# Performance work log

Measured on AMD Instinct MI355X. Metric: run time of the kernel, lower is better.

Reference implementation:

```python
import jax, jax.numpy as jnp
from jax import lax
import numpy as np

B, T, V, E, H, D, NH = 64, 121, 100000, 300, 256, 512, 3  # D = 2*H (BiLSTM output)


def setup_inputs() -> dict:
    key = jax.random.key(0)
    ks = jax.random.split(key, 24)
    s = 0.05
    n = lambda k, shp: (jax.random.normal(k, shp, dtype=jnp.float32) * s)
    return {
        'tokens': jax.random.randint(ks[0], (B, T), 0, V, dtype=jnp.int32),
        'lengths': jax.random.randint(ks[1], (B,), 1, T + 1, dtype=jnp.int32),
        'emb': n(ks[2], (V, E)),
        'Wx_f': n(ks[3], (E, 4 * H)), 'Wh_f': n(ks[4], (H, 4 * H)), 'b_f': jnp.zeros((4 * H,), jnp.float32),
        'Wx_b': n(ks[5], (E, 4 * H)), 'Wh_b': n(ks[6], (H, 4 * H)), 'b_b': jnp.zeros((4 * H,), jnp.float32),
        'W1': n(ks[7], (4 * D, E)), 'b1': jnp.zeros((E,), jnp.float32),
        'W2': n(ks[8], (E, 1)), 'b2': jnp.zeros((1,), jnp.float32),
        'Wr': n(ks[9], (D, D)), 'Ur': n(ks[10], (D, D)), 'br': jnp.zeros((D,), jnp.float32),
        'Wc': n(ks[11], (D, D)), 'Uc': n(ks[12], (D, D)), 'bc': jnp.zeros((D,), jnp.float32),
        'q': n(ks[13], (B, D)),
        'W_hops': n(ks[14], (NH, 3 * D, D)), 'b_hops': jnp.zeros((NH, D), jnp.float32),
        'Wo': n(ks[15], (2 * D, 1)), 'bo': jnp.zeros((1,), jnp.float32),
    }


def _lstm(x, Wx, Wh, b, reverse=False):
    # x: [B, T, E] -> outputs [B, T, H]
    xp = jnp.einsum('bte,eg->btg', x, Wx) + b  # precompute input projections
    def cell(carry, xt):
        h, c = carry
        g = xt + h @ Wh
        i, f, gg, o = jnp.split(g, 4, axis=-1)
        c = jax.nn.sigmoid(f) * c + jax.nn.sigmoid(i) * jnp.tanh(gg)
        h = jax.nn.sigmoid(o) * jnp.tanh(c)
        return (h, c), h
    h0 = jnp.zeros((x.shape[0], Wh.shape[0]), x.dtype)
    (_, _), ys = lax.scan(cell, (h0, h0), jnp.swapaxes(xp, 0, 1), reverse=reverse)
    return jnp.swapaxes(ys, 0, 1)


def _attention(facts, q, m, mask, W1, b1, W2, b2):
    # facts [B,T,D]; q,m [B,D] -> softmax attention [B,T] (masked by length)
    qe, me = q[:, None, :], m[:, None, :]
    z = jnp.concatenate([facts * qe, facts * me, jnp.abs(facts - qe), jnp.abs(facts - me)], axis=-1)
    h = jnp.tanh(jnp.einsum('btf,fe->bte', z, W1) + b1)
    s = (jnp.einsum('bte,eo->bto', h, W2) + b2)[..., 0]  # [B,T]
    s = jnp.where(mask, s, jnp.float32(-1e9))
    return jax.nn.softmax(s, axis=1)


def _attn_gru(facts, g, Wr, Ur, br, Wc, Uc, bc):
    # attention-gated GRU over time; episode = final state [B,D]
    def cell(h, inp):
        x, gt = inp
        r = jax.nn.sigmoid(x @ Wr + h @ Ur + br)
        hc = jnp.tanh(x @ Wc + r * (h @ Uc) + bc)
        h = gt[:, None] * hc + (1.0 - gt[:, None]) * h
        return h, None
    h0 = jnp.zeros_like(facts[:, 0])
    h, _ = lax.scan(cell, h0, (jnp.swapaxes(facts, 0, 1), g.T))
    return h


def reference(tokens, lengths, emb, Wx_f, Wh_f, b_f, Wx_b, Wh_b, b_b,
              W1, b1, W2, b2, Wr, Ur, br, Wc, Uc, bc, q,
              W_hops, b_hops, Wo, bo):
    x = emb[tokens]  # [B,T,E]
    fwd = _lstm(x, Wx_f, Wh_f, b_f, reverse=False)
    bwd = _lstm(x, Wx_b, Wh_b, b_b, reverse=True)
    facts = jnp.concatenate([fwd, bwd], axis=-1)  # [B,T,D]
    mask = jnp.arange(T)[None, :] < lengths[:, None]
    m = q
    for i in range(NH):  # episodic memory hops (attention weights shared across hops)
        a = _attention(facts, q, m, mask, W1, b1, W2, b2)
        ep = _attn_gru(facts, a, Wr, Ur, br, Wc, Uc, bc)
        m = jax.nn.relu(jnp.concatenate([m, ep, q], axis=1) @ W_hops[i] + b_hops[i])
    out = jax.nn.sigmoid(jnp.concatenate([m, q], axis=1) @ Wo + bo)
    return jnp.squeeze(out, axis=-1)  # [B]
```

## Files before the change

kernel.cpp:

```cpp
#include <hip/hip_runtime.h>

constexpr int B  = 64;
constexpr int T  = 121;
constexpr int E  = 300;
constexpr int Ep = 320;
constexpr int H  = 256;
constexpr int G4 = 1024;
constexpr int D  = 512;
constexpr int NH = 3;
constexpr int BT = B * T;
constexpr int Mp = 7808;

using short8 = __attribute__((ext_vector_type(8))) short;
using f32x4  = __attribute__((ext_vector_type(4))) float;

__device__ __forceinline__ float sigmoidf(float x) { return 1.0f / (1.0f + __expf(-x)); }
__device__ __forceinline__ float tanhf_fast(float x) {
  float e = __expf(2.0f * x);
  return 1.0f - 2.0f / (e + 1.0f);
}
__device__ __forceinline__ unsigned bf16rne(float x) {
  unsigned u = __float_as_uint(x);
  return (u + 0x7fffu + ((u >> 16) & 1u)) >> 16;
}
__device__ __forceinline__ float bf_lo(unsigned u) { return __uint_as_float(u << 16); }
__device__ __forceinline__ float bf_hi(unsigned u) { return __uint_as_float(u & 0xffff0000u); }
__device__ __forceinline__ float bfu(unsigned short u) { return __uint_as_float(((unsigned)u) << 16); }

__global__ void k_pack_lstm(const float* __restrict__ Wh,
                            uint4* __restrict__ PAQ, uint4* __restrict__ PBQ) {
  int idx = blockIdx.x * 256 + threadIdx.x;
  int k4 = idx >> 8, j = idx & 255;
  int k = 4 * k4;
  uint4 a, bq;
  const float* r0 = Wh + (size_t)(k + 0) * G4;
  const float* r1 = Wh + (size_t)(k + 1) * G4;
  const float* r2 = Wh + (size_t)(k + 2) * G4;
  const float* r3 = Wh + (size_t)(k + 3) * G4;
  a.x  = bf16rne(r0[j]) | (bf16rne(r0[j + 256]) << 16);
  a.y  = bf16rne(r1[j]) | (bf16rne(r1[j + 256]) << 16);
  a.z  = bf16rne(r2[j]) | (bf16rne(r2[j + 256]) << 16);
  a.w  = bf16rne(r3[j]) | (bf16rne(r3[j + 256]) << 16);
  bq.x = bf16rne(r0[j + 512]) | (bf16rne(r0[j + 768]) << 16);
  bq.y = bf16rne(r1[j + 512]) | (bf16rne(r1[j + 768]) << 16);
  bq.z = bf16rne(r2[j + 512]) | (bf16rne(r2[j + 768]) << 16);
  bq.w = bf16rne(r3[j + 512]) | (bf16rne(r3[j + 768]) << 16);
  PAQ[idx] = a;
  PBQ[idx] = bq;
}

__global__ void k_packT(const float* __restrict__ W, unsigned short* __restrict__ WT,
                        int Ksrc, int Nsrc, int stride, int Kpad) {
  int idx = blockIdx.x * 256 + threadIdx.x;
  int n = idx / Kpad, k = idx - n * Kpad;
  float v = (k < Ksrc && n < Nsrc) ? W[(size_t)k * stride + n] : 0.0f;
  WT[idx] = (unsigned short)bf16rne(v);
}

__global__ void k_gather(const int* __restrict__ tokens, const float* __restrict__ emb,
                         unsigned short* __restrict__ xh) {
  int bt = blockIdx.x;
  int tok = tokens[bt];
  const float* src = emb + (size_t)tok * E;
  unsigned short* dst = xh + (size_t)bt * Ep;
  for (int e = threadIdx.x; e < Ep; e += 256)
    dst[e] = (e < E) ? (unsigned short)bf16rne(src[e]) : (unsigned short)0;
}

__global__ __launch_bounds__(256) void k_gemm_mfma(
    const unsigned short* __restrict__ A1, const unsigned short* __restrict__ B1, int K1, int lda1,
    const unsigned short* __restrict__ A2, const unsigned short* __restrict__ B2, int K2, int lda2,
    const float* __restrict__ bias, const float* __restrict__ Cin,
    float* __restrict__ C, int Nreal, int Cstride)
{
  __shared__ unsigned short As[128][40];
  __shared__ unsigned short Bs[64][40];
  int tid = threadIdx.x;
  int l = tid & 63, w = tid >> 6;
  int row0 = blockIdx.y * 128, col0 = blockIdx.x * 64;
  int lrow = l & 15, lk = (l >> 4) * 8, lq = (l >> 4) * 4;
  int ar = tid >> 1, asg = (tid & 1) * 16;
  int br = tid >> 2, bsg = (tid & 3) * 8;
  f32x4 acc[2][4] = {};
#pragma unroll 1
  for (int pass = 0; pass < 2; ++pass) {
    const unsigned short* A  = pass ? A2 : A1;
    const unsigned short* Bt = pass ? B2 : B1;
    int K   = pass ? K2 : K1;
    int lda = pass ? lda2 : lda1;
    if (K == 0) break;
    for (int k0 = 0; k0 < K; k0 += 32) {
      const uint4* ga = (const uint4*)(A + (size_t)(row0 + ar) * lda + k0 + asg);
      uint4 a0 = ga[0], a1 = ga[1];
      uint4 b0 = *(const uint4*)(Bt + (size_t)(col0 + br) * K + k0 + bsg);
      __syncthreads();
      *(uint4*)&As[ar][asg]     = a0;
      *(uint4*)&As[ar][asg + 8] = a1;
      *(uint4*)&Bs[br][bsg]     = b0;
      __syncthreads();
      short8 av[2], bv[4];
#pragma unroll
      for (int f = 0; f < 2; ++f)
        av[f] = *(const short8*)&As[w * 32 + f * 16 + lrow][lk];
#pragma unroll
      for (int fc = 0; fc < 4; ++fc)
        bv[fc] = *(const short8*)&Bs[fc * 16 + lrow][lk];
#pragma unroll
      for (int f = 0; f < 2; ++f)
#pragma unroll
        for (int fc = 0; fc < 4; ++fc)
          acc[f][fc] = __builtin_amdgcn_mfma_f32_16x16x32_bf16(av[f], bv[fc], acc[f][fc], 0, 0, 0);
    }
  }
#pragma unroll
  for (int f = 0; f < 2; ++f) {
#pragma unroll
    for (int fc = 0; fc < 4; ++fc) {
      int c = col0 + fc * 16 + lrow;
      if (c < Nreal) {
        float bb = bias ? bias[c] : 0.0f;
#pragma unroll
        for (int i = 0; i < 4; ++i) {
          int r = row0 + w * 32 + f * 16 + lq + i;
          if (r < BT) {
            float v = acc[f][fc][i] + bb;
            if (Cin) v += Cin[(size_t)r * Cstride + c];
            C[(size_t)r * Cstride + c] = v;
          }
        }
      }
    }
  }
}

__global__ __launch_bounds__(512) void k_lstm(
    const float* __restrict__ xp_f, const float* __restrict__ xp_b,
    const uint4* __restrict__ PAQ_f, const uint4* __restrict__ PBQ_f,
    const uint4* __restrict__ PAQ_b, const uint4* __restrict__ PBQ_b,
    const int* __restrict__ lengths, unsigned short* __restrict__ factsh)
{
  int b = blockIdx.x;
  int dir = blockIdx.y;
  const float* xp = dir ? xp_b : xp_f;
  const uint4* PAQ = dir ? PAQ_b : PAQ_f;
  const uint4* PBQ = dir ? PBQ_b : PBQ_f;
  int tid = threadIdx.x;
  int j = tid & 255, half = tid >> 8;
  __shared__ float hs[H];
  __shared__ float4 red[512];
  hs[j] = 0.0f;
  float c = 0.0f, h = 0.0f;
  int nsteps = dir ? T : lengths[b];
  const uint4* pa = PAQ + (size_t)(half * 32) * 256 + j;
  const uint4* pb = PBQ + (size_t)(half * 32) * 256 + j;
  const float4* hs4 = reinterpret_cast<const float4*>(hs) + half * 32;
  __syncthreads();
  for (int s = 0; s < nsteps; ++s) {
    int t = dir ? (T - 1 - s) : s;
    float g0 = 0.f, g1 = 0.f, g2 = 0.f, g3 = 0.f;
#pragma unroll 4
    for (int k4 = 0; k4 < 32; ++k4) {
      uint4 a  = pa[(size_t)k4 * 256];
      uint4 bq = pb[(size_t)k4 * 256];
      float4 hv = hs4[k4];
      g0 = fmaf(hv.x, bf_lo(a.x), g0);  g1 = fmaf(hv.x, bf_hi(a.x), g1);
      g2 = fmaf(hv.x, bf_lo(bq.x), g2); g3 = fmaf(hv.x, bf_hi(bq.x), g3);
      g0 = fmaf(hv.y, bf_lo(a.y), g0);  g1 = fmaf(hv.y, bf_hi(a.y), g1);
      g2 = fmaf(hv.y, bf_lo(bq.y), g2); g3 = fmaf(hv.y, bf_hi(bq.y), g3);
      g0 = fmaf(hv.z, bf_lo(a.z), g0);  g1 = fmaf(hv.z, bf_hi(a.z), g1);
      g2 = fmaf(hv.z, bf_lo(bq.z), g2); g3 = fmaf(hv.z, bf_hi(bq.z), g3);
      g0 = fmaf(hv.w, bf_lo(a.w), g0);  g1 = fmaf(hv.w, bf_hi(a.w), g1);
      g2 = fmaf(hv.w, bf_lo(bq.w), g2); g3 = fmaf(hv.w, bf_hi(bq.w), g3);
    }
    red[tid] = make_float4(g0, g1, g2, g3);
    __syncthreads();
    if (half == 0) {
      float4 o = red[tid + 256];
      const float* xrow = xp + (size_t)(b * T + t) * G4;
      g0 += o.x + xrow[j];
      g1 += o.y + xrow[j + 256];
      g2 += o.z + xrow[j + 512];
      g3 += o.w + xrow[j + 768];
      float ig = sigmoidf(g0);
      float fg = sigmoidf(g1);
      float gg = tanhf_fast(g2);
      float og = sigmoidf(g3);
      c = fg * c + ig * gg;
      h = og * tanhf_fast(c);
      hs[j] = h;
      factsh[(size_t)(b * T + t) * D + dir * H + j] = (unsigned short)bf16rne(h);
    }
    __syncthreads();
  }
}

__global__ void k_buildz(const unsigned short* __restrict__ factsh, const float* __restrict__ v,
                         unsigned short* __restrict__ za, unsigned short* __restrict__ zb) {
  int bt = blockIdx.x;
  int b = bt / T;
  int d = threadIdx.x;
  float f = bfu(factsh[(size_t)bt * D + d]);
  float vv = v[(size_t)b * D + d];
  za[(size_t)bt * D + d] = (unsigned short)bf16rne(f * vv);
  zb[(size_t)bt * D + d] = (unsigned short)bf16rne(fabsf(f - vv));
}

__global__ void k_score(const float* __restrict__ att_h, const float* __restrict__ W2,
                        const float* __restrict__ b2, float* __restrict__ s) {
  int bt = blockIdx.x;
  int tid = threadIdx.x;
  float acc = 0.f;
  for (int e = tid; e < E; e += 64)
    acc += tanhf_fast(att_h[(size_t)bt * E + e]) * W2[e];
  for (int off = 32; off > 0; off >>= 1) acc += __shfl_down(acc, off);
  if (tid == 0) s[bt] = acc + b2[0];
}

__global__ void k_softmax(const float* __restrict__ s, const int* __restrict__ lengths,
                          float* __restrict__ a) {
  int b = blockIdx.x;
  int t = threadIdx.x;
  int len = lengths[b];
  __shared__ float wred[2];
  float val = -1e30f;
  if (t < T) val = (t < len) ? s[b * T + t] : -1e9f;
  float mx = val;
  for (int off = 32; off > 0; off >>= 1) mx = fmaxf(mx, __shfl_xor(mx, off));
  int wid = t >> 6, lane = t & 63;
  if (lane == 0) wred[wid] = mx;
  __syncthreads();
  mx = fmaxf(wred[0], wred[1]);
  __syncthreads();
  float e = (t < T && t < len) ? __expf(val - mx) : 0.0f;
  float sum = e;
  for (int off = 32; off > 0; off >>= 1) sum += __shfl_xor(sum, off);
  if (lane == 0) wred[wid] = sum;
  __syncthreads();
  float tot = wred[0] + wred[1];
  if (t < T) a[b * T + t] = e / tot;
}

__global__ void k_zero(int* __restrict__ p, int n) {
  int i = blockIdx.x * blockDim.x + threadIdx.x;
  if (i < n) p[i] = 0;
}
__global__ void k_ginit(unsigned short* __restrict__ Hb0) {
  Hb0[blockIdx.x * 512 + threadIdx.x] = 0;
}

__global__ __launch_bounds__(256) void k_gru_hop(
    const unsigned short* __restrict__ URCT,
    unsigned short* __restrict__ Hb,
    float* __restrict__ ep,
    const float* __restrict__ xr, const float* __restrict__ xc,
    const float* __restrict__ br, const float* __restrict__ bc,
    const float* __restrict__ att, int* __restrict__ syncA)
{
  __shared__ unsigned short Wl[64 * 512];
  const int tid = threadIdx.x;
  const int bi  = blockIdx.x;
  const int j0  = bi * 32;
  const int l = tid & 63, w = tid >> 6;
  const int lrow = l & 15, g = l >> 4;
  const int lq = g * 4;

  for (int it = tid; it < 64 * 64; it += 256) {
    int row = it >> 6, unit = it & 63;
    int grow = (row < 32) ? (j0 + row) : (512 + j0 + row - 32);
    uint4 v = *(const uint4*)(URCT + (size_t)grow * 512 + unit * 8);
    *(uint4*)&Wl[row * 512 + ((unit ^ (row & 7)) * 8)] = v;
  }
  __syncthreads();

  float h[2][4] = {};
  float brj[2], bcj[2];
#pragma unroll
  for (int fc = 0; fc < 2; ++fc) {
    brj[fc] = br[j0 + fc * 16 + lrow];
    bcj[fc] = bc[j0 + fc * 16 + lrow];
  }

  for (int t = 0; t < T; ++t) {
    const unsigned short* Hin = Hb + (size_t)(t & 1) * (B * D);
    unsigned short*      Hout = Hb + (size_t)((t + 1) & 1) * (B * D);
    uint4 a[16];
#pragma unroll
    for (int c = 0; c < 16; ++c)
      a[c] = *(const uint4*)(Hin + (size_t)(w * 16 + lrow) * D + c * 32 + g * 8);
    float xrv[2][4], xcv[2][4], gv[4];
#pragma unroll
    for (int i = 0; i < 4; ++i) {
      int b = w * 16 + lq + i;
      gv[i] = att[b * T + t];
#pragma unroll
      for (int fc = 0; fc < 2; ++fc) {
        size_t base = (size_t)(b * T + t) * D + j0 + fc * 16 + lrow;
        xrv[fc][i] = xr[base];
        xcv[fc][i] = xc[base];
      }
    }
    f32x4 acc[4] = {};
#pragma unroll
    for (int c = 0; c < 16; ++c) {
      short8 av = *(const short8*)&a[c];
#pragma unroll
      for (int fc = 0; fc < 4; ++fc) {
        int row = fc * 16 + lrow;
        short8 bv = *(const short8*)&Wl[row * 512 + (((c * 4 + g) ^ (row & 7)) * 8)];
        acc[fc] = __builtin_amdgcn_mfma_f32_16x16x32_bf16(av, bv, acc[fc], 0, 0, 0);
      }
    }
#pragma unroll
    for (int fc = 0; fc < 2; ++fc) {
#pragma unroll
      for (int i = 0; i < 4; ++i) {
        int b = w * 16 + lq + i;
        float r  = sigmoidf(xrv[fc][i] + acc[fc][i] + brj[fc]);
        float hc = tanhf_fast(xcv[fc][i] + r * acc[fc + 2][i] + bcj[fc]);
        float hn = gv[i] * hc + (1.f - gv[i]) * h[fc][i];
        h[fc][i] = hn;
        Hout[(size_t)b * D + j0 + fc * 16 + lrow] = (unsigned short)bf16rne(hn);
      }
    }
    __syncthreads();
    if (tid == 0) {
      __threadfence();
      atomicAdd(&syncA[t], 1);
      while (__hip_atomic_load(&syncA[t], __ATOMIC_RELAXED, __HIP_MEMORY_SCOPE_AGENT) < 16)
        __builtin_amdgcn_s_sleep(1);
    }
    __syncthreads();
    __threadfence();
  }
#pragma unroll
  for (int fc = 0; fc < 2; ++fc)
#pragma unroll
    for (int i = 0; i < 4; ++i) {
      int b = w * 16 + lq + i;
      ep[(size_t)b * D + j0 + fc * 16 + lrow] = h[fc][i];
    }
}

__global__ __launch_bounds__(512) void k_hop(
    const float* __restrict__ m_in, const float* __restrict__ ep,
    const float* __restrict__ q, const float* __restrict__ Whop,
    const float* __restrict__ bhop, float* __restrict__ m_out)
{
  int b = blockIdx.x, j = threadIdx.x;
  __shared__ float av[3 * D];
  av[j]         = m_in[(size_t)b * D + j];
  av[D + j]     = ep[(size_t)b * D + j];
  av[2 * D + j] = q[(size_t)b * D + j];
  __syncthreads();
  float acc = bhop[j];
#pragma unroll 4
  for (int k = 0; k < 3 * D; ++k)
    acc = fmaf(av[k], Whop[(size_t)k * D + j], acc);
  m_out[(size_t)b * D + j] = fmaxf(acc, 0.0f);
}

__global__ void k_out(const float* __restrict__ m, const float* __restrict__ q,
                      const float* __restrict__ Wo, const float* __restrict__ bo,
                      float* __restrict__ out)
{
  int b = blockIdx.x, tid = threadIdx.x;
  float acc = 0.f;
  for (int k = tid; k < D; k += 256)
    acc += m[(size_t)b * D + k] * Wo[k] + q[(size_t)b * D + k] * Wo[D + k];
  for (int off = 32; off > 0; off >>= 1) acc += __shfl_down(acc, off);
  __shared__ float red[4];
  int wid = tid >> 6, lane = tid & 63;
  if (lane == 0) red[wid] = acc;
  __syncthreads();
  if (tid == 0) {
    float tot = red[0] + red[1] + red[2] + red[3];
    out[b] = 1.0f / (1.0f + __expf(-(tot + bo[0])));
  }
}

extern "C" void kernel_launch(void* const* d_in, const int* in_sizes, int n_in,
                              void* d_out, int out_size, void* d_ws, size_t ws_size,
                              hipStream_t stream)
{
  const int*   tokens  = (const int*)d_in[0];
  const int*   lengths = (const int*)d_in[1];
  const float* emb     = (const float*)d_in[2];
  const float* Wx_f    = (const float*)d_in[3];
  const float* Wh_f    = (const float*)d_in[4];
  const float* b_f     = (const float*)d_in[5];
  const float* Wx_b    = (const float*)d_in[6];
  const float* Wh_b    = (const float*)d_in[7];
  const float* b_b     = (const float*)d_in[8];
  const float* W1      = (const float*)d_in[9];
  const float* b1      = (const float*)d_in[10];
  const float* W2      = (const float*)d_in[11];
  const float* b2      = (const float*)d_in[12];
  const float* Wr      = (const float*)d_in[13];
  const float* Ur      = (const float*)d_in[14];
  const float* br      = (const float*)d_in[15];
  const float* Wc      = (const float*)d_in[16];
  const float* Uc      = (const float*)d_in[17];
  const float* bc      = (const float*)d_in[18];
  const float* q       = (const float*)d_in[19];
  const float* W_hops  = (const float*)d_in[20];
  const float* b_hops  = (const float*)d_in[21];
  const float* Wo      = (const float*)d_in[22];
  const float* bo      = (const float*)d_in[23];
  float* ws = (float*)d_ws;

  float* p = ws;
  unsigned short* xh = (unsigned short*)p;  p += (size_t)Mp * Ep / 2;
  float* xp_f   = p;  p += (size_t)BT * G4;
  float* xp_b   = p;  p += (size_t)BT * G4;
  unsigned short* factsh = (unsigned short*)p;  p += (size_t)Mp * D / 2;
  float* att_h  = p;  p += (size_t)BT * E;
  float* part0  = p;  p += (size_t)BT * E;
  float* scores = p;  p += BT;
  float* att    = p;  p += BT;
  float* m0     = p;  p += (size_t)B * D;
  float* m1     = p;  p += (size_t)B * D;
  float* epb    = p;  p += (size_t)B * D;
  unsigned short* Hb = (unsigned short*)p;  p += (size_t)2 * B * D / 2;
  int* syncA    = (int*)p;  p += 3 * 128;
  uint4* PAQ_f  = (uint4*)p;  p += (size_t)(H / 4) * 256 * 4;
  uint4* PBQ_f  = (uint4*)p;  p += (size_t)(H / 4) * 256 * 4;
  uint4* PAQ_b  = (uint4*)p;  p += (size_t)(H / 4) * 256 * 4;
  uint4* PBQ_b  = (uint4*)p;  p += (size_t)(H / 4) * 256 * 4;
  unsigned short* WxT_f = (unsigned short*)p;  p += (size_t)G4 * Ep / 2;
  unsigned short* WxT_b = (unsigned short*)p;  p += (size_t)G4 * Ep / 2;
  unsigned short* WrT   = (unsigned short*)p;  p += (size_t)D * D / 2;
  unsigned short* WcT   = (unsigned short*)p;  p += (size_t)D * D / 2;
  unsigned short* URCT  = (unsigned short*)p;  p += (size_t)(2 * D) * D / 2;
  unsigned short* W1T[4];
  for (int c = 0; c < 4; ++c) { W1T[c] = (unsigned short*)p; p += (size_t)Ep * D / 2; }
  float* xr = xp_f;
  float* xc = xp_f + (size_t)BT * D;
  unsigned short* za = (unsigned short*)xp_b;
  unsigned short* zb = (unsigned short*)xp_b + (size_t)Mp * D;

  k_zero<<<1, 384, 0, stream>>>(syncA, 3 * 128);
  k_pack_lstm<<<(H / 4) * 256 / 256, 256, 0, stream>>>(Wh_f, PAQ_f, PBQ_f);
  k_pack_lstm<<<(H / 4) * 256 / 256, 256, 0, stream>>>(Wh_b, PAQ_b, PBQ_b);
  k_packT<<<G4 * Ep / 256, 256, 0, stream>>>(Wx_f, WxT_f, E, G4, G4, Ep);
  k_packT<<<G4 * Ep / 256, 256, 0, stream>>>(Wx_b, WxT_b, E, G4, G4, Ep);
  k_packT<<<D * D / 256, 256, 0, stream>>>(Wr, WrT, D, D, D, D);
  k_packT<<<D * D / 256, 256, 0, stream>>>(Wc, WcT, D, D, D, D);
  k_packT<<<D * D / 256, 256, 0, stream>>>(Ur, URCT, D, D, D, D);
  k_packT<<<D * D / 256, 256, 0, stream>>>(Uc, URCT + (size_t)D * D, D, D, D, D);
  for (int c = 0; c < 4; ++c)
    k_packT<<<Ep * D / 256, 256, 0, stream>>>(W1 + (size_t)c * D * E, W1T[c], D, E, E, D);

  k_gather<<<BT, 256, 0, stream>>>(tokens, emb, xh);
  k_gemm_mfma<<<dim3(G4 / 64, Mp / 128), 256, 0, stream>>>(
      xh, WxT_f, Ep, Ep, nullptr, nullptr, 0, 0, b_f, nullptr, xp_f, G4, G4);
  k_gemm_mfma<<<dim3(G4 / 64, Mp / 128), 256, 0, stream>>>(
      xh, WxT_b, Ep, Ep, nullptr, nullptr, 0, 0, b_b, nullptr, xp_b, G4, G4);
  k_lstm<<<dim3(B, 2), 512, 0, stream>>>(xp_f, xp_b, PAQ_f, PBQ_f, PAQ_b, PBQ_b, lengths, factsh);
  k_gemm_mfma<<<dim3(D / 64, Mp / 128), 256, 0, stream>>>(
      factsh, WrT, D, D, nullptr, nullptr, 0, 0, nullptr, nullptr, xr, D, D);
  k_gemm_mfma<<<dim3(D / 64, Mp / 128), 256, 0, stream>>>(
      factsh, WcT, D, D, nullptr, nullptr, 0, 0, nullptr, nullptr, xc, D, D);
  k_buildz<<<BT, 512, 0, stream>>>(factsh, q, za, zb);
  k_gemm_mfma<<<dim3(Ep / 64, Mp / 128), 256, 0, stream>>>(
      za, W1T[0], D, D, zb, W1T[2], D, D, b1, nullptr, part0, E, E);

  const float* m_in = q;
  float* mb[2] = {m0, m1};
  for (int i = 0; i < NH; ++i) {
    k_buildz<<<BT, 512, 0, stream>>>(factsh, m_in, za, zb);
    k_gemm_mfma<<<dim3(Ep / 64, Mp / 128), 256, 0, stream>>>(
        za, W1T[1], D, D, zb, W1T[3], D, D, nullptr, part0, att_h, E, E);
    k_score<<<BT, 64, 0, stream>>>(att_h, W2, b2, scores);
    k_softmax<<<B, 128, 0, stream>>>(scores, lengths, att);
    k_ginit<<<B * D / 512, 512, 0, stream>>>(Hb);
    k_gru_hop<<<16, 256, 0, stream>>>(URCT, Hb, epb, xr, xc, br, bc, att, syncA + i * 128);
    k_hop<<<B, 512, 0, stream>>>(m_in, epb, q,
                                 W_hops + (size_t)i * 3 * D * D, b_hops + (size_t)i * D,
                                 mb[i & 1]);
    m_in = mb[i & 1];
  }
  k_out<<<B, 256, 0, stream>>>(m_in, q, Wo, bo, (float*)d_out);
}
```

Measured before the change: 3.419 ms.

## Halve GRU grid-barrier blocks, prefetch next-step inputs, pack xr/xc as bf16

The recurrent attention-GRU kernel now runs on 8 blocks of 512 threads instead of 16 blocks of 256. Each block holds two 32-column weight slices in 128 KB of dynamic LDS, so the per-timestep atomic grid barrier waits on half as many blocks. The next timestep's gate and input projections are loaded before the MFMA work so their latency overlaps the compute. A new pre-pass packs the fp32 xr and xc projections into bf16 pairs, halving the bytes read per step at the cost of some precision and one extra kernel launch. The large dynamic LDS allocation limits occupancy and depends on the device allowing more than 64 KB per block.

```diff
diff --git a/kernel.cpp b/kernel.cpp
--- a/kernel.cpp
+++ b/kernel.cpp
@@ -55,6 +55,12 @@
   int n = idx / Kpad, k = idx - n * Kpad;
   float v = (k < Ksrc && n < Nsrc) ? W[(size_t)k * stride + n] : 0.0f;
   WT[idx] = (unsigned short)bf16rne(v);
+}
+
+__global__ void k_packxrc(const float* xr, const float* xc, unsigned* XRC) {
+  size_t i = (size_t)blockIdx.x * 512 + threadIdx.x;
+  float r = xr[i], c = xc[i];
+  XRC[i] = bf16rne(r) | (bf16rne(c) << 16);
 }
 
 __global__ void k_gather(const int* __restrict__ tokens, const float* __restrict__ emb,
@@ -248,31 +254,35 @@
   Hb0[blockIdx.x * 512 + threadIdx.x] = 0;
 }
 
-__global__ __launch_bounds__(256) void k_gru_hop(
+__global__ __launch_bounds__(512) void k_gru_hop(
     const unsigned short* __restrict__ URCT,
     unsigned short* __restrict__ Hb,
     float* __restrict__ ep,
-    const float* __restrict__ xr, const float* __restrict__ xc,
+    const unsigned* __restrict__ XRC,
     const float* __restrict__ br, const float* __restrict__ bc,
     const float* __restrict__ att, int* __restrict__ syncA)
 {
-  __shared__ unsigned short Wl[64 * 512];
+  extern __shared__ unsigned short Wl[];
   const int tid = threadIdx.x;
   const int bi  = blockIdx.x;
-  const int j0  = bi * 32;
-  const int l = tid & 63, w = tid >> 6;
+  const int w   = tid >> 6;
+  const int s   = w >> 2;
+  const int wb  = w & 3;
+  const int l   = tid & 63;
   const int lrow = l & 15, g = l >> 4;
-  const int lq = g * 4;
-
-  for (int it = tid; it < 64 * 64; it += 256) {
-    int row = it >> 6, unit = it & 63;
-    int grow = (row < 32) ? (j0 + row) : (512 + j0 + row - 32);
+  const int lq  = g * 4;
+  const int j0  = bi * 64 + s * 32;
+  const unsigned short* WlS = Wl + s * 64 * 512;
+
+  for (int it = tid; it < 128 * 64; it += 512) {
+    int row128 = it >> 6, unit = it & 63;
+    int sl = row128 >> 6, row = row128 & 63;
+    int jb = bi * 64 + sl * 32;
+    int grow = (row < 32) ? (jb + row) : (512 + jb + row - 32);
     uint4 v = *(const uint4*)(URCT + (size_t)grow * 512 + unit * 8);
-    *(uint4*)&Wl[row * 512 + ((unit ^ (row & 7)) * 8)] = v;
-  }
-  __syncthreads();
-
-  float h[2][4] = {};
+    *(uint4*)&Wl[sl * 64 * 512 + row * 512 + ((unit ^ (row & 7)) * 8)] = v;
+  }
+
   float brj[2], bcj[2];
 #pragma unroll
   for (int fc = 0; fc < 2; ++fc) {
@@ -280,23 +290,36 @@
     bcj[fc] = bc[j0 + fc * 16 + lrow];
   }
 
+  unsigned xq[2][4];
+  float gv[4];
+#pragma unroll
+  for (int i = 0; i < 4; ++i) {
+    int b = wb * 16 + lq + i;
+    gv[i] = att[b * T];
+#pragma unroll
+    for (int fc = 0; fc < 2; ++fc)
+      xq[fc][i] = XRC[(size_t)(b * T) * D + j0 + fc * 16 + lrow];
+  }
+  __syncthreads();
+
+  float h[2][4] = {};
   for (int t = 0; t < T; ++t) {
     const unsigned short* Hin = Hb + (size_t)(t & 1) * (B * D);
     unsigned short*      Hout = Hb + (size_t)((t + 1) & 1) * (B * D);
     uint4 a[16];
 #pragma unroll
     for (int c = 0; c < 16; ++c)
-      a[c] = *(const uint4*)(Hin + (size_t)(w * 16 + lrow) * D + c * 32 + g * 8);
-    float xrv[2][4], xcv[2][4], gv[4];
-#pragma unroll
-    for (int i = 0; i < 4; ++i) {
-      int b = w * 16 + lq + i;
-      gv[i] = att[b * T + t];
-#pragma unroll
-      for (int fc = 0; fc < 2; ++fc) {
-        size_t base = (size_t)(b * T + t) * D + j0 + fc * 16 + lrow;
-        xrv[fc][i] = xr[base];
-        xcv[fc][i] = xc[base];
+      a[c] = *(const uint4*)(Hin + (size_t)(wb * 16 + lrow) * D + c * 32 + g * 8);
+    unsigned xqn[2][4] = {};
+    float gvn[4] = {};
+    if (t + 1 < T) {
+#pragma unroll
+      for (int i = 0; i < 4; ++i) {
+        int b = wb * 16 + lq + i;
+        gvn[i] = att[b * T + t + 1];
+#pragma unroll
+        for (int fc = 0; fc < 2; ++fc)
+          xqn[fc][i] = XRC[(size_t)(b * T + t + 1) * D + j0 + fc * 16 + lrow];
       }
     }
     f32x4 acc[4] = {};
@@ -306,7 +329,7 @@
 #pragma unroll
       for (int fc = 0; fc < 4; ++fc) {
         int row = fc * 16 + lrow;
-        short8 bv = *(const short8*)&Wl[row * 512 + (((c * 4 + g) ^ (row & 7)) * 8)];
+        short8 bv = *(const short8*)&WlS[row * 512 + (((c * 4 + g) ^ (row & 7)) * 8)];
         acc[fc] = __builtin_amdgcn_mfma_f32_16x16x32_bf16(av, bv, acc[fc], 0, 0, 0);
       }
     }
@@ -314,9 +337,9 @@
     for (int fc = 0; fc < 2; ++fc) {
 #pragma unroll
       for (int i = 0; i < 4; ++i) {
-        int b = w * 16 + lq + i;
-        float r  = sigmoidf(xrv[fc][i] + acc[fc][i] + brj[fc]);
-        float hc = tanhf_fast(xcv[fc][i] + r * acc[fc + 2][i] + bcj[fc]);
+        int b = wb * 16 + lq + i;
+        float r  = sigmoidf(bf_lo(xq[fc][i]) + acc[fc][i] + brj[fc]);
+        float hc = tanhf_fast(bf_hi(xq[fc][i]) + r * acc[fc + 2][i] + bcj[fc]);
         float hn = gv[i] * hc + (1.f - gv[i]) * h[fc][i];
         h[fc][i] = hn;
         Hout[(size_t)b * D + j0 + fc * 16 + lrow] = (unsigned short)bf16rne(hn);
@@ -326,17 +349,23 @@
     if (tid == 0) {
       __threadfence();
       atomicAdd(&syncA[t], 1);
-      while (__hip_atomic_load(&syncA[t], __ATOMIC_RELAXED, __HIP_MEMORY_SCOPE_AGENT) < 16)
+      while (__hip_atomic_load(&syncA[t], __ATOMIC_RELAXED, __HIP_MEMORY_SCOPE_AGENT) < 8)
         __builtin_amdgcn_s_sleep(1);
     }
     __syncthreads();
     __threadfence();
+#pragma unroll
+    for (int i = 0; i < 4; ++i) {
+      gv[i] = gvn[i];
+#pragma unroll
+      for (int fc = 0; fc < 2; ++fc) xq[fc][i] = xqn[fc][i];
+    }
   }
 #pragma unroll
   for (int fc = 0; fc < 2; ++fc)
 #pragma unroll
     for (int i = 0; i < 4; ++i) {
-      int b = w * 16 + lq + i;
+      int b = wb * 16 + lq + i;
       ep[(size_t)b * D + j0 + fc * 16 + lrow] = h[fc][i];
     }
 }
@@ -435,6 +464,7 @@
   for (int c = 0; c < 4; ++c) { W1T[c] = (unsigned short*)p; p += (size_t)Ep * D / 2; }
   float* xr = xp_f;
   float* xc = xp_f + (size_t)BT * D;
+  unsigned* XRC = (unsigned*)xr;
   unsigned short* za = (unsigned short*)xp_b;
   unsigned short* zb = (unsigned short*)xp_b + (size_t)Mp * D;
 
@@ -460,6 +490,7 @@
       factsh, WrT, D, D, nullptr, nullptr, 0, 0, nullptr, nullptr, xr, D, D);
   k_gemm_mfma<<<dim3(D / 64, Mp / 128), 256, 0, stream>>>(
       factsh, WcT, D, D, nullptr, nullptr, 0, 0, nullptr, nullptr, xc, D, D);
+  k_packxrc<<<BT * D / 512, 512, 0, stream>>>(xr, xc, XRC);
   k_buildz<<<BT, 512, 0, stream>>>(factsh, q, za, zb);
   k_gemm_mfma<<<dim3(Ep / 64, Mp / 128), 256, 0, stream>>>(
       za, W1T[0], D, D, zb, W1T[2], D, D, b1, nullptr, part0, E, E);
@@ -473,7 +504,8 @@
     k_score<<<BT, 64, 0, stream>>>(att_h, W2, b2, scores);
     k_softmax<<<B, 128, 0, stream>>>(scores, lengths, att);
     k_ginit<<<B * D / 512, 512, 0, stream>>>(Hb);
-    k_gru_hop<<<16, 256, 0, stream>>>(URCT, Hb, epb, xr, xc, br, bc, att, syncA + i * 128);
+    k_gru_hop<<<8, 512, 128 * 512 * sizeof(unsigned short), stream>>>(
+        URCT, Hb, epb, XRC, br, bc, att, syncA + i * 128);
     k_hop<<<B, 512, 0, stream>>>(m_in, epb, q,
                                  W_hops + (size_t)i * 3 * D * D, b_hops + (size_t)i * D,
                                  mb[i & 1]);
```

After: 4.403 ms. 28.8% more time.

## Split GRU hop across 32 blocks, pack xr/xc to bf16, prefetch next step

Applied to the files above, without the earlier changes.

The persistent GRU recurrence now runs on 32 blocks, each owning 16 hidden units instead of 32. This halves each block's per-step MFMA chain and its LDS weight footprint. The precomputed input projections xr and xc are packed in place into one bf16 pair per element, so each step does a single 32-bit load. Those loads and the attention gate are fetched one step ahead to hide their latency behind the matmul. The trade-offs are bf16 rounding of the projections and a grid barrier that now waits on twice as many blocks.

```diff
diff --git a/kernel.cpp b/kernel.cpp
--- a/kernel.cpp
+++ b/kernel.cpp
@@ -55,6 +55,12 @@
   int n = idx / Kpad, k = idx - n * Kpad;
   float v = (k < Ksrc && n < Nsrc) ? W[(size_t)k * stride + n] : 0.0f;
   WT[idx] = (unsigned short)bf16rne(v);
+}
+
+__global__ void k_packxrc(const float* xr, const float* xc, unsigned* XRC) {
+  size_t i = (size_t)blockIdx.x * 512 + threadIdx.x;
+  float r = xr[i], c = xc[i];
+  XRC[i] = bf16rne(r) | (bf16rne(c) << 16);
 }
 
 __global__ void k_gather(const int* __restrict__ tokens, const float* __restrict__ emb,
@@ -252,34 +258,40 @@
     const unsigned short* __restrict__ URCT,
     unsigned short* __restrict__ Hb,
     float* __restrict__ ep,
-    const float* __restrict__ xr, const float* __restrict__ xc,
+    const unsigned* __restrict__ XRC,
     const float* __restrict__ br, const float* __restrict__ bc,
     const float* __restrict__ att, int* __restrict__ syncA)
 {
-  __shared__ unsigned short Wl[64 * 512];
+  __shared__ unsigned short Wl[32 * 512];
   const int tid = threadIdx.x;
   const int bi  = blockIdx.x;
-  const int j0  = bi * 32;
-  const int l = tid & 63, w = tid >> 6;
+  const int j0  = bi * 16;
+  const int w   = tid >> 6;
+  const int l   = tid & 63;
   const int lrow = l & 15, g = l >> 4;
-  const int lq = g * 4;
-
-  for (int it = tid; it < 64 * 64; it += 256) {
+  const int lq  = g * 4;
+  const int j   = j0 + lrow;
+
+  for (int it = tid; it < 32 * 64; it += 256) {
     int row = it >> 6, unit = it & 63;
-    int grow = (row < 32) ? (j0 + row) : (512 + j0 + row - 32);
+    int grow = (row < 16) ? (j0 + row) : (512 + j0 + row - 16);
     uint4 v = *(const uint4*)(URCT + (size_t)grow * 512 + unit * 8);
     *(uint4*)&Wl[row * 512 + ((unit ^ (row & 7)) * 8)] = v;
   }
-  __syncthreads();
-
-  float h[2][4] = {};
-  float brj[2], bcj[2];
-#pragma unroll
-  for (int fc = 0; fc < 2; ++fc) {
-    brj[fc] = br[j0 + fc * 16 + lrow];
-    bcj[fc] = bc[j0 + fc * 16 + lrow];
-  }
-
+
+  const float brj = br[j], bcj = bc[j];
+
+  unsigned xq[4];
+  float gv[4];
+#pragma unroll
+  for (int i = 0; i < 4; ++i) {
+    int b = w * 16 + lq + i;
+    gv[i] = att[b * T];
+    xq[i] = XRC[(size_t)(b * T) * D + j];
+  }
+  __syncthreads();
+
+  float h[4] = {};
   for (int t = 0; t < T; ++t) {
     const unsigned short* Hin = Hb + (size_t)(t & 1) * (B * D);
     unsigned short*      Hout = Hb + (size_t)((t + 1) & 1) * (B * D);
@@ -287,58 +299,53 @@
 #pragma unroll
     for (int c = 0; c < 16; ++c)
       a[c] = *(const uint4*)(Hin + (size_t)(w * 16 + lrow) * D + c * 32 + g * 8);
-    float xrv[2][4], xcv[2][4], gv[4];
-#pragma unroll
-    for (int i = 0; i < 4; ++i) {
-      int b = w * 16 + lq + i;
-      gv[i] = att[b * T + t];
-#pragma unroll
-      for (int fc = 0; fc < 2; ++fc) {
-        size_t base = (size_t)(b * T + t) * D + j0 + fc * 16 + lrow;
-        xrv[fc][i] = xr[base];
-        xcv[fc][i] = xc[base];
+    unsigned xqn[4] = {};
+    float gvn[4] = {};
+    if (t + 1 < T) {
+#pragma unroll
+      for (int i = 0; i < 4; ++i) {
+        int b = w * 16 + lq + i;
+        gvn[i] = att[b * T + t + 1];
+        xqn[i] = XRC[(size_t)(b * T + t + 1) * D + j];
       }
     }
-    f32x4 acc[4] = {};
+    f32x4 acc[2] = {};
 #pragma unroll
     for (int c = 0; c < 16; ++c) {
       short8 av = *(const short8*)&a[c];
 #pragma unroll
-      for (int fc = 0; fc < 4; ++fc) {
+      for (int fc = 0; fc < 2; ++fc) {
         int row = fc * 16 + lrow;
         short8 bv = *(const short8*)&Wl[row * 512 + (((c * 4 + g) ^ (row & 7)) * 8)];
         acc[fc] = __builtin_amdgcn_mfma_f32_16x16x32_bf16(av, bv, acc[fc], 0, 0, 0);
       }
     }
 #pragma unroll
-    for (int fc = 0; fc < 2; ++fc) {
-#pragma unroll
-      for (int i = 0; i < 4; ++i) {
-        int b = w * 16 + lq + i;
-        float r  = sigmoidf(xrv[fc][i] + acc[fc][i] + brj[fc]);
-        float hc = tanhf_fast(xcv[fc][i] + r * acc[fc + 2][i] + bcj[fc]);
-        float hn = gv[i] * hc + (1.f - gv[i]) * h[fc][i];
-        h[fc][i] = hn;
-        Hout[(size_t)b * D + j0 + fc * 16 + lrow] = (unsigned short)bf16rne(hn);
-      }
+    for (int i = 0; i < 4; ++i) {
+      int b = w * 16 + lq + i;
+      float r  = sigmoidf(bf_lo(xq[i]) + acc[0][i] + brj);
+      float hc = tanhf_fast(bf_hi(xq[i]) + r * acc[1][i] + bcj);
+      float hn = gv[i] * hc + (1.f - gv[i]) * h[i];
+      h[i] = hn;
+      Hout[(size_t)b * D + j] = (unsigned short)bf16rne(hn);
     }
     __syncthreads();
     if (tid == 0) {
       __threadfence();
       atomicAdd(&syncA[t], 1);
-      while (__hip_atomic_load(&syncA[t], __ATOMIC_RELAXED, __HIP_MEMORY_SCOPE_AGENT) < 16)
+      while (__hip_atomic_load(&syncA[t], __ATOMIC_RELAXED, __HIP_MEMORY_SCOPE_AGENT) < 32)
         __builtin_amdgcn_s_sleep(1);
     }
     __syncthreads();
     __threadfence();
-  }
-#pragma unroll
-  for (int fc = 0; fc < 2; ++fc)
-#pragma unroll
-    for (int i = 0; i < 4; ++i) {
-      int b = w * 16 + lq + i;
-      ep[(size_t)b * D + j0 + fc * 16 + lrow] = h[fc][i];
-    }
+#pragma unroll
+    for (int i = 0; i < 4; ++i) { gv[i] = gvn[i]; xq[i] = xqn[i]; }
+  }
+#pragma unroll
+  for (int i = 0; i < 4; ++i) {
+    int b = w * 16 + lq + i;
+    ep[(size_t)b * D + j] = h[i];
+  }
 }
 
 __global__ __launch_bounds__(512) void k_hop(
@@ -435,6 +442,7 @@
   for (int c = 0; c < 4; ++c) { W1T[c] = (unsigned short*)p; p += (size_t)Ep * D / 2; }
   float* xr = xp_f;
   float* xc = xp_f + (size_t)BT * D;
+  unsigned* XRC = (unsigned*)xr;
   unsigned short* za = (unsigned short*)xp_b;
   unsigned short* zb = (unsigned short*)xp_b + (size_t)Mp * D;
 
@@ -460,6 +468,7 @@
       factsh, WrT, D, D, nullptr, nullptr, 0, 0, nullptr, nullptr, xr, D, D);
   k_gemm_mfma<<<dim3(D / 64, Mp / 128), 256, 0, stream>>>(
       factsh, WcT, D, D, nullptr, nullptr, 0, 0, nullptr, nullptr, xc, D, D);
+  k_packxrc<<<BT * D / 512, 512, 0, stream>>>(xr, xc, XRC);
   k_buildz<<<BT, 512, 0, stream>>>(factsh, q, za, zb);
   k_gemm_mfma<<<dim3(Ep / 64, Mp / 128), 256, 0, stream>>>(
       za, W1T[0], D, D, zb, W1T[2], D, D, b1, nullptr, part0, E, E);
@@ -473,7 +482,7 @@
     k_score<<<BT, 64, 0, stream>>>(att_h, W2, b2, scores);
     k_softmax<<<B, 128, 0, stream>>>(scores, lengths, att);
     k_ginit<<<B * D / 512, 512, 0, stream>>>(Hb);
-    k_gru_hop<<<16, 256, 0, stream>>>(URCT, Hb, epb, xr, xc, br, bc, att, syncA + i * 128);
+    k_gru_hop<<<32, 256, 0, stream>>>(URCT, Hb, epb, XRC, br, bc, att, syncA + i * 128);
     k_hop<<<B, 512, 0, stream>>>(m_in, epb, q,
                                  W_hops + (size_t)i * 3 * D * D, b_hops + (size_t)i * D,
                                  mb[i & 1]);
```

New measurement: 3.830 ms. +12.0%, slower.
